# Performance work log

Measured on AMD Instinct MI355X. Metric: run time of the kernel, lower is better.

The kernel has to match this reference:

```python
import jax, jax.numpy as jnp
import numpy as np

EPS = 1e-5

def _layernorm(x, w, b):
    mu = jnp.mean(x, axis=-1, keepdims=True)
    var = jnp.var(x, axis=-1, keepdims=True)
    return (x - mu) * jax.lax.rsqrt(var + EPS) * w + b

def setup_inputs() -> dict:
    key = jax.random.key(0)
    ks = jax.random.split(key, 9)
    b, s, dim = 4, 4096, 2048
    m, n, dim_ctx = 8, 64, 1024
    heads, dim_head = 8, 64
    inner = heads * dim_head
    x = jax.random.normal(ks[0], (b, s, dim), dtype=jnp.float32)
    context = jax.random.normal(ks[1], (b, m, n, dim_ctx), dtype=jnp.float32)
    media_locations = jax.random.randint(ks[2], (b, s), 0, m, dtype=jnp.int64)
    scale = 0.02
    norm_w = jnp.ones((dim,), jnp.float32)
    norm_b = jnp.zeros((dim,), jnp.float32)
    normc_w = jnp.ones((dim_ctx,), jnp.float32)
    normc_b = jnp.zeros((dim_ctx,), jnp.float32)
    Wq = jax.random.normal(ks[3], (dim, inner), jnp.float32) * scale
    Wkv = jax.random.normal(ks[4], (dim_ctx, 2 * inner), jnp.float32) * scale
    Wout = jax.random.normal(ks[5], (inner, dim), jnp.float32) * scale
    return {"x": x, "context": context, "media_locations": media_locations,
            "norm_w": norm_w, "norm_b": norm_b, "normc_w": normc_w, "normc_b": normc_b,
            "Wq": Wq, "Wkv": Wkv, "Wout": Wout}

def reference(x, context, media_locations, norm_w, norm_b, normc_w, normc_b, Wq, Wkv, Wout):
    heads, dim_head = 8, 64
    b, m, n, dc = context.shape
    scale = dim_head ** -0.5
    xn = _layernorm(x, norm_w, norm_b)                       # [b,s,dim]
    ctx = _layernorm(context.reshape(b, m * n, dc), normc_w, normc_b)  # [b,mn,dc]
    q = xn @ Wq                                              # [b,s,inner]
    kv = ctx @ Wkv                                           # [b,mn,2*inner]
    k, v = jnp.split(kv, 2, axis=-1)
    def to_heads(t):
        return t.reshape(t.shape[0], t.shape[1], heads, dim_head).transpose(0, 2, 1, 3)
    q, k, v = to_heads(q), to_heads(k), to_heads(v)          # [b,h,*,d]
    sim = jnp.einsum('bhid,bhjd->bhij', q, k) * scale        # [b,h,s,mn]
    # image-causal mask: kv token j belongs to image j//n; query i may only
    # attend to image media_locations[b,i] (negative index => all masked)
    j_img = jnp.arange(m * n) // n                           # [mn]
    allowed = (media_locations[:, :, None] == j_img[None, None, :]) & (media_locations[:, :, None] >= 0)
    sim = jnp.where(allowed[:, None, :, :], sim, -jnp.inf)
    attn = jax.nn.softmax(sim, axis=-1)
    out = jnp.einsum('bhij,bhjd->bhid', attn, v)             # [b,h,s,d]
    out = out.transpose(0, 2, 1, 3).reshape(b, x.shape[1], heads * dim_head)
    return out @ Wout
```

## Files before the change

### kernel.cpp

```cpp
#include <hip/hip_runtime.h>

typedef unsigned short u16;
typedef unsigned int u32;
typedef __attribute__((ext_vector_type(8))) short short8;
typedef __attribute__((ext_vector_type(4))) short short4_t;
typedef __attribute__((ext_vector_type(4))) float f32x4;

__device__ __forceinline__ float bf2f(u16 u){ return __uint_as_float(((u32)u)<<16); }
__device__ __forceinline__ u16 f2bf(float f){ u32 x = __float_as_uint(f); return (u16)((x + 0x7FFFu + ((x>>16)&1u)) >> 16); }

#define OFF_FLAG   ((size_t)0)
#define OFF_COUNTS ((size_t)256)
#define OFF_LISTS  ((size_t)4096)
#define OFF_XN     ((size_t)(1<<20))
#define OFF_CTXN   (OFF_XN    + (size_t)67108864)
#define OFF_WQT    (OFF_CTXN  + (size_t)4194304)
#define OFF_WKVT   (OFF_WQT   + (size_t)2097152)
#define OFF_WOUTT  (OFF_WKVT  + (size_t)2097152)
#define OFF_Q      (OFF_WOUTT + (size_t)2097152)
#define OFF_KV     (OFF_Q     + (size_t)16777216)
#define OFF_ATTN   (OFF_KV    + (size_t)4194304)
#define OFF_VT     (OFF_ATTN  + (size_t)16777216)
#define WS_NEEDED  (OFF_VT    + (size_t)2097152)

__global__ void prep_kernel(const int* __restrict__ ml32, int* __restrict__ flag, int* __restrict__ counts){
  int t = threadIdx.x;
  if (t < 32) counts[t] = 0;
  __shared__ int nz;
  if (t == 0) nz = 0;
  __syncthreads();
  if (t < 128 && ml32[2*t+1] != 0) atomicAdd(&nz, 1);
  __syncthreads();
  if (t == 0) flag[0] = (nz == 0) ? 1 : 0;
}

template<int D>
__global__ __launch_bounds__(256) void ln_bf16(const float* __restrict__ x, const float* __restrict__ w,
                                               const float* __restrict__ b, u16* __restrict__ out){
  constexpr int VEC = D/256;
  int row = blockIdx.x;
  const float* xr = x + (size_t)row*D;
  int tid = threadIdx.x;
  float v[VEC];
  #pragma unroll
  for (int i=0;i<VEC;i+=4){
    f32x4 f = *(const f32x4*)(xr + tid*VEC + i);
    v[i]=f[0]; v[i+1]=f[1]; v[i+2]=f[2]; v[i+3]=f[3];
  }
  float s=0.f, sq=0.f;
  #pragma unroll
  for (int i=0;i<VEC;++i){ s += v[i]; sq += v[i]*v[i]; }
  #pragma unroll
  for (int off=32;off;off>>=1){ s += __shfl_xor(s,off,64); sq += __shfl_xor(sq,off,64); }
  __shared__ float red[8];
  int lane = tid&63, wid = tid>>6;
  if (lane==0){ red[wid]=s; red[4+wid]=sq; }
  __syncthreads();
  s  = red[0]+red[1]+red[2]+red[3];
  sq = red[4]+red[5]+red[6]+red[7];
  float mu = s/(float)D;
  float var = sq/(float)D - mu*mu;
  float rs = rsqrtf(var + 1e-5f);
  u16 o[VEC];
  #pragma unroll
  for (int i=0;i<VEC;i+=4){
    f32x4 wv = *(const f32x4*)(w + tid*VEC + i);
    f32x4 bv = *(const f32x4*)(b + tid*VEC + i);
    #pragma unroll
    for (int u=0;u<4;++u) o[i+u] = f2bf((v[i+u]-mu)*rs*wv[u] + bv[u]);
  }
  if constexpr (VEC==8) *(short8*)(out + (size_t)row*D + tid*8) = *(short8*)o;
  else                  *(short4_t*)(out + (size_t)row*D + tid*4) = *(short4_t*)o;
}

__global__ __launch_bounds__(256) void transpose_all(const float* __restrict__ Wq, const float* __restrict__ Wkv,
                                                     const float* __restrict__ Wout, u16* __restrict__ WqT,
                                                     u16* __restrict__ WkvT, u16* __restrict__ WoutT){
  __shared__ float t[32][33];
  int id = blockIdx.x;
  const float* in; u16* out; int K, N, tile, tx_n;
  if (id < 1024)      { in=Wq;   out=WqT;   K=2048; N=512;  tile=id;      tx_n=16; }
  else if (id < 2048) { in=Wkv;  out=WkvT;  K=1024; N=1024; tile=id-1024; tx_n=32; }
  else                { in=Wout; out=WoutT; K=512;  N=2048; tile=id-2048; tx_n=64; }
  int n0 = (tile % tx_n)*32, k0 = (tile / tx_n)*32;
  int tx = threadIdx.x & 31, ty = threadIdx.x >> 5;
  #pragma unroll
  for (int r=0;r<32;r+=8) t[ty+r][tx] = in[(size_t)(k0+ty+r)*N + n0+tx];
  __syncthreads();
  #pragma unroll
  for (int r=0;r<32;r+=8) out[(size_t)(n0+ty+r)*K + k0+tx] = f2bf(t[tx][ty+r]);
}

__global__ __launch_bounds__(256) void transpose_v(const u16* __restrict__ kvb, u16* __restrict__ vt){
  int h = blockIdx.x, bl = blockIdx.y;
  __shared__ u16 t[64][72];
  int tid = threadIdx.x;
  const u16* src = kvb + (size_t)(bl*64)*1024 + 512 + h*64;
  #pragma unroll
  for (int i=0;i<2;++i){
    int idx = i*2048 + tid*8;
    int key = idx>>6, d = idx&63;
    *(short8*)&t[key][d] = *(const short8*)(src + (size_t)key*1024 + d);
  }
  __syncthreads();
  u16* dst = vt + (size_t)(bl*8+h)*4096;
  #pragma unroll
  for (int i=0;i<2;++i){
    int idx = i*2048 + tid*8;
    int d = idx>>6, k0 = idx&63;
    u16 tmp[8];
    #pragma unroll
    for (int u=0;u<8;++u) tmp[u] = t[k0+u][d];
    *(short8*)(dst + d*64 + k0) = *(short8*)tmp;
  }
}

template<int MODE>
__global__ __launch_bounds__(256) void gemm_bt(const u16* __restrict__ A, const u16* __restrict__ B,
                                               void* __restrict__ Cv, int M, int N, int K){
  __shared__ __align__(16) u16 lds[2][2][128*32];
  int tid = threadIdx.x, lane = tid&63, wid = tid>>6;
  int nbn = N>>7;
  int nwg = gridDim.x;
  int wg = blockIdx.x;
  int cpx = nwg>>3;
  wg = (wg&7)*cpx + (wg>>3);
  int brow = wg/nbn, bcol = wg%nbn;

  auto stage = [&](int buf, int kt){
    #pragma unroll
    for (int i=0;i<2;++i){
      int cb = i*256 + wid*64;
      int c  = cb + lane;
      int row = c>>2, kc = c&3;
      const u16* ga = A + (size_t)(brow*128+row)*K + kt*32 + kc*8;
      __builtin_amdgcn_global_load_lds((const __attribute__((address_space(1))) u32*)ga,
          (__attribute__((address_space(3))) u32*)&lds[buf][0][cb*8], 16, 0, 0);
      const u16* gb = B + (size_t)(bcol*128+row)*K + kt*32 + kc*8;
      __builtin_amdgcn_global_load_lds((const __attribute__((address_space(1))) u32*)gb,
          (__attribute__((address_space(3))) u32*)&lds[buf][1][cb*8], 16, 0, 0);
    }
  };

  int wm = wid>>1, wn = wid&1;
  f32x4 acc[4][4] = {};
  int nkt = K>>5;
  stage(0,0);
  __syncthreads();
  for (int kt=0; kt<nkt; ++kt){
    int cur = kt&1;
    if (kt+1<nkt) stage(cur^1, kt+1);
    short8 af[4], bfr[4];
    int r = lane&15, kq = lane>>4;
    #pragma unroll
    for (int mi=0;mi<4;++mi) af[mi]  = *(const short8*)&lds[cur][0][(wm*64+mi*16+r)*32 + kq*8];
    #pragma unroll
    for (int ni=0;ni<4;++ni) bfr[ni] = *(const short8*)&lds[cur][1][(wn*64+ni*16+r)*32 + kq*8];
    #pragma unroll
    for (int mi=0;mi<4;++mi)
      #pragma unroll
      for (int ni=0;ni<4;++ni)
        acc[mi][ni] = __builtin_amdgcn_mfma_f32_16x16x32_bf16(af[mi], bfr[ni], acc[mi][ni], 0,0,0);
    __syncthreads();
  }
  int r4 = (lane>>4)*4, cc = lane&15;
  #pragma unroll
  for (int mi=0;mi<4;++mi)
    #pragma unroll
    for (int ni=0;ni<4;++ni)
      #pragma unroll
      for (int rr=0;rr<4;++rr){
        int row = brow*128 + wm*64 + mi*16 + r4 + rr;
        int col = bcol*128 + wn*64 + ni*16 + cc;
        float val = acc[mi][ni][rr];
        if (MODE==2) val *= 0.125f;
        if (MODE)  ((u16*)Cv)[(size_t)row*N+col] = f2bf(val);
        else       ((float*)Cv)[(size_t)row*N+col] = val;
      }
}

__global__ void bucket_kernel(const int* __restrict__ ml32, const int* __restrict__ flag,
                              int* __restrict__ counts, int* __restrict__ lists){
  int i = blockIdx.x*256 + threadIdx.x;
  int loc = flag[0] ? ml32[2*i] : ml32[i];
  int bl = (i>>12)*8 + loc;
  int pos = atomicAdd(&counts[bl], 1);
  lists[bl*4096 + pos] = i & 4095;
}

__global__ __launch_bounds__(512) void attn_mfma5(const u16* __restrict__ qb, const u16* __restrict__ kvb,
                                                  const u16* __restrict__ vt, u16* __restrict__ ob,
                                                  const int* __restrict__ counts, const int* __restrict__ lists){
  int bl = blockIdx.y, chunk = blockIdx.x;
  int cnt = counts[bl];
  int q0 = chunk*32;
  if (q0 >= cnt) return;
  int b = bl>>3, loc = bl&7;
  int tid = threadIdx.x, lane = tid&63, h = tid>>6;
  __shared__ u16 qs[32][520];
  int r = lane&15, g = lane>>4;

  const u16* kbase = kvb + (size_t)(b*512 + loc*64)*1024 + h*64;
  short8 kfr[4][2];
  #pragma unroll
  for (int nt=0;nt<4;++nt){
    const u16* krow = kbase + (size_t)(nt*16 + r)*1024;
    kfr[nt][0] = *(const short8*)(krow + g*8);
    kfr[nt][1] = *(const short8*)(krow + 32 + g*8);
  }
  const u16* vbase = vt + (size_t)(bl*8 + h)*4096;
  short8 vf[2][4];
  #pragma unroll
  for (int nt=0;nt<4;++nt){
    const u16* vrow = vbase + (size_t)(nt*16 + r)*64;
    vf[0][nt] = *(const short8*)(vrow + g*8);
    vf[1][nt] = *(const short8*)(vrow + 32 + g*8);
  }

  const u16* qbase = qb + (size_t)(b*4096)*512;
  #pragma unroll
  for (int p=0;p<4;++p){
    int c = p*512 + tid;
    int row = c>>6, cc = c&63;
    int qq = (q0 + row < cnt) ? lists[bl*4096 + q0 + row] : -1;
    if (qq >= 0)
      *(short8*)&qs[row][cc*8] = *(const short8*)(qbase + (size_t)qq*512 + cc*8);
  }
  __syncthreads();

  short8 qf[2][2];
  #pragma unroll
  for (int mt=0;mt<2;++mt){
    qf[mt][0] = *(const short8*)&qs[mt*16+r][h*64 + g*8];
    qf[mt][1] = *(const short8*)&qs[mt*16+r][h*64 + 32 + g*8];
  }

  f32x4 acc[2][4] = {};
  #pragma unroll
  for (int mt=0;mt<2;++mt)
    #pragma unroll
    for (int nt=0;nt<4;++nt){
      acc[mt][nt] = __builtin_amdgcn_mfma_f32_16x16x32_bf16(qf[mt][0], kfr[nt][0], acc[mt][nt], 0,0,0);
      acc[mt][nt] = __builtin_amdgcn_mfma_f32_16x16x32_bf16(qf[mt][1], kfr[nt][1], acc[mt][nt], 0,0,0);
    }

  #pragma unroll
  for (int mt=0;mt<2;++mt){
    #pragma unroll
    for (int rr=0;rr<4;++rr){
      float m = fmaxf(fmaxf(acc[mt][0][rr], acc[mt][1][rr]), fmaxf(acc[mt][2][rr], acc[mt][3][rr]));
      #pragma unroll
      for (int off=1;off<16;off<<=1) m = fmaxf(m, __shfl_xor(m, off));
      float e0 = __expf(acc[mt][0][rr]-m), e1 = __expf(acc[mt][1][rr]-m);
      float e2 = __expf(acc[mt][2][rr]-m), e3 = __expf(acc[mt][3][rr]-m);
      float sum = (e0+e1)+(e2+e3);
      #pragma unroll
      for (int off=1;off<16;off<<=1) sum += __shfl_xor(sum, off);
      float rs = 1.0f/sum;
      int row = mt*16 + g*4 + rr;
      qs[row][h*64 +  0 + r] = f2bf(e0*rs);
      qs[row][h*64 + 16 + r] = f2bf(e1*rs);
      qs[row][h*64 + 32 + r] = f2bf(e2*rs);
      qs[row][h*64 + 48 + r] = f2bf(e3*rs);
    }
  }

  f32x4 oacc[2][4] = {};
  #pragma unroll
  for (int mt=0;mt<2;++mt){
    short8 pa0 = *(const short8*)&qs[mt*16 + r][h*64 + g*8];
    short8 pa1 = *(const short8*)&qs[mt*16 + r][h*64 + 32 + g*8];
    #pragma unroll
    for (int nt=0;nt<4;++nt){
      oacc[mt][nt] = __builtin_amdgcn_mfma_f32_16x16x32_bf16(pa0, vf[0][nt], oacc[mt][nt], 0,0,0);
      oacc[mt][nt] = __builtin_amdgcn_mfma_f32_16x16x32_bf16(pa1, vf[1][nt], oacc[mt][nt], 0,0,0);
    }
  }

  #pragma unroll
  for (int mt=0;mt<2;++mt)
    #pragma unroll
    for (int rr=0;rr<4;++rr){
      int row = mt*16 + g*4 + rr;
      #pragma unroll
      for (int nt=0;nt<4;++nt)
        qs[row][h*64 + nt*16 + r] = f2bf(oacc[mt][nt][rr]);
    }
  __syncthreads();

  #pragma unroll
  for (int p=0;p<4;++p){
    int c = p*512 + tid;
    int row = c>>6, cc = c&63;
    int qq = (q0 + row < cnt) ? lists[bl*4096 + q0 + row] : -1;
    if (qq >= 0)
      *(short8*)(ob + ((size_t)(b*4096) + qq)*512 + cc*8) = *(const short8*)&qs[row][cc*8];
  }
}

extern "C" void kernel_launch(void* const* d_in, const int* in_sizes, int n_in,
                              void* d_out, int out_size, void* d_ws, size_t ws_size,
                              hipStream_t stream) {
  const float* x    = (const float*)d_in[0];
  const float* ctx  = (const float*)d_in[1];
  const int*   ml   = (const int*)d_in[2];
  const float* nw   = (const float*)d_in[3];
  const float* nb   = (const float*)d_in[4];
  const float* ncw  = (const float*)d_in[5];
  const float* ncb  = (const float*)d_in[6];
  const float* Wq   = (const float*)d_in[7];
  const float* Wkv  = (const float*)d_in[8];
  const float* Wout = (const float*)d_in[9];
  float* out = (float*)d_out;
  char* ws = (char*)d_ws;
  if (ws_size < WS_NEEDED) return;

  int* flag   = (int*)(ws + OFF_FLAG);
  int* counts = (int*)(ws + OFF_COUNTS);
  int* lists  = (int*)(ws + OFF_LISTS);
  u16* xn     = (u16*)(ws + OFF_XN);
  u16* ctxn   = (u16*)(ws + OFF_CTXN);
  u16* WqT    = (u16*)(ws + OFF_WQT);
  u16* WkvT   = (u16*)(ws + OFF_WKVT);
  u16* WoutT  = (u16*)(ws + OFF_WOUTT);
  u16* qbuf   = (u16*)(ws + OFF_Q);
  u16* kvbuf  = (u16*)(ws + OFF_KV);
  u16* attn_o = (u16*)(ws + OFF_ATTN);
  u16* vtbuf  = (u16*)(ws + OFF_VT);

  prep_kernel<<<1,256,0,stream>>>(ml, flag, counts);
  ln_bf16<2048><<<16384,256,0,stream>>>(x,   nw,  nb,  xn);
  ln_bf16<1024><<<2048, 256,0,stream>>>(ctx, ncw, ncb, ctxn);
  transpose_all<<<3072, 256,0,stream>>>(Wq, Wkv, Wout, WqT, WkvT, WoutT);
  gemm_bt<2><<<512, 256,0,stream>>>(xn,   WqT,  qbuf,  16384, 512,  2048);
  gemm_bt<1><<<128, 256,0,stream>>>(ctxn, WkvT, kvbuf, 2048,  1024, 1024);
  transpose_v<<<dim3(8,32),256,0,stream>>>(kvbuf, vtbuf);
  bucket_kernel<<<64,256,0,stream>>>(ml, flag, counts, lists);
  attn_mfma5<<<dim3(128,32),512,0,stream>>>(qbuf, kvbuf, vtbuf, attn_o, counts, lists);
  gemm_bt<0><<<2048,256,0,stream>>>(attn_o, WoutT, out, 16384, 2048, 512);
}
```

Baseline: 241.5 us.

## Merge small prep kernels into fewer launches and aggregate bucket atomics in LDS

Combines the context layernorm, weight transposes and flag/count init into one kernel, merges the Q and KV GEMMs into a single launch, and fuses the V transpose with bucketing. Bucketing now counts per block in shared memory before doing one global atomic per bucket. This cuts the number of launches from ten to six and removes tail bubbles from tiny grids. The cost is divergent block roles and dependence on launch ordering for the counts reset.

```diff
diff --git a/kernel.cpp b/kernel.cpp
--- a/kernel.cpp
+++ b/kernel.cpp
@@ -23,21 +23,9 @@
 #define OFF_VT     (OFF_ATTN  + (size_t)16777216)
 #define WS_NEEDED  (OFF_VT    + (size_t)2097152)
 
-__global__ void prep_kernel(const int* __restrict__ ml32, int* __restrict__ flag, int* __restrict__ counts){
-  int t = threadIdx.x;
-  if (t < 32) counts[t] = 0;
-  __shared__ int nz;
-  if (t == 0) nz = 0;
-  __syncthreads();
-  if (t < 128 && ml32[2*t+1] != 0) atomicAdd(&nz, 1);
-  __syncthreads();
-  if (t == 0) flag[0] = (nz == 0) ? 1 : 0;
-}
-
-template<int D>
-__global__ __launch_bounds__(256) void ln_bf16(const float* __restrict__ x, const float* __restrict__ w,
-                                               const float* __restrict__ b, u16* __restrict__ out){
-  constexpr int VEC = D/256;
+__global__ __launch_bounds__(256) void ln_x(const float* __restrict__ x, const float* __restrict__ w,
+                                            const float* __restrict__ b, u16* __restrict__ out){
+  constexpr int D = 2048, VEC = 8;
   int row = blockIdx.x;
   const float* xr = x + (size_t)row*D;
   int tid = threadIdx.x;
@@ -69,60 +57,72 @@
     #pragma unroll
     for (int u=0;u<4;++u) o[i+u] = f2bf((v[i+u]-mu)*rs*wv[u] + bv[u]);
   }
-  if constexpr (VEC==8) *(short8*)(out + (size_t)row*D + tid*8) = *(short8*)o;
-  else                  *(short4_t*)(out + (size_t)row*D + tid*4) = *(short4_t*)o;
-}
-
-__global__ __launch_bounds__(256) void transpose_all(const float* __restrict__ Wq, const float* __restrict__ Wkv,
-                                                     const float* __restrict__ Wout, u16* __restrict__ WqT,
-                                                     u16* __restrict__ WkvT, u16* __restrict__ WoutT){
+  *(short8*)(out + (size_t)row*D + tid*8) = *(short8*)o;
+}
+
+__global__ __launch_bounds__(256) void ctx_prep(const float* __restrict__ ctx, const float* __restrict__ ncw,
+                                                const float* __restrict__ ncb, u16* __restrict__ ctxn,
+                                                const float* __restrict__ Wq, const float* __restrict__ Wkv,
+                                                const float* __restrict__ Wout, u16* __restrict__ WqT,
+                                                u16* __restrict__ WkvT, u16* __restrict__ WoutT,
+                                                const int* __restrict__ ml32, int* __restrict__ flag,
+                                                int* __restrict__ counts){
+  int id = blockIdx.x, tid = threadIdx.x;
+  __shared__ float red[8];
   __shared__ float t[32][33];
-  int id = blockIdx.x;
-  const float* in; u16* out; int K, N, tile, tx_n;
-  if (id < 1024)      { in=Wq;   out=WqT;   K=2048; N=512;  tile=id;      tx_n=16; }
-  else if (id < 2048) { in=Wkv;  out=WkvT;  K=1024; N=1024; tile=id-1024; tx_n=32; }
-  else                { in=Wout; out=WoutT; K=512;  N=2048; tile=id-2048; tx_n=64; }
-  int n0 = (tile % tx_n)*32, k0 = (tile / tx_n)*32;
-  int tx = threadIdx.x & 31, ty = threadIdx.x >> 5;
-  #pragma unroll
-  for (int r=0;r<32;r+=8) t[ty+r][tx] = in[(size_t)(k0+ty+r)*N + n0+tx];
-  __syncthreads();
-  #pragma unroll
-  for (int r=0;r<32;r+=8) out[(size_t)(n0+ty+r)*K + k0+tx] = f2bf(t[tx][ty+r]);
-}
-
-__global__ __launch_bounds__(256) void transpose_v(const u16* __restrict__ kvb, u16* __restrict__ vt){
-  int h = blockIdx.x, bl = blockIdx.y;
-  __shared__ u16 t[64][72];
-  int tid = threadIdx.x;
-  const u16* src = kvb + (size_t)(bl*64)*1024 + 512 + h*64;
-  #pragma unroll
-  for (int i=0;i<2;++i){
-    int idx = i*2048 + tid*8;
-    int key = idx>>6, d = idx&63;
-    *(short8*)&t[key][d] = *(const short8*)(src + (size_t)key*1024 + d);
-  }
-  __syncthreads();
-  u16* dst = vt + (size_t)(bl*8+h)*4096;
-  #pragma unroll
-  for (int i=0;i<2;++i){
-    int idx = i*2048 + tid*8;
-    int d = idx>>6, k0 = idx&63;
-    u16 tmp[8];
-    #pragma unroll
-    for (int u=0;u<8;++u) tmp[u] = t[k0+u][d];
-    *(short8*)(dst + d*64 + k0) = *(short8*)tmp;
+  __shared__ int nz;
+  if (id < 2048){
+    constexpr int D = 1024;
+    const float* xr = ctx + (size_t)id*D;
+    f32x4 f = *(const f32x4*)(xr + tid*4);
+    float s = f[0]+f[1]+f[2]+f[3];
+    float sq = f[0]*f[0]+f[1]*f[1]+f[2]*f[2]+f[3]*f[3];
+    #pragma unroll
+    for (int off=32;off;off>>=1){ s += __shfl_xor(s,off,64); sq += __shfl_xor(sq,off,64); }
+    int lane = tid&63, wid = tid>>6;
+    if (lane==0){ red[wid]=s; red[4+wid]=sq; }
+    __syncthreads();
+    s  = red[0]+red[1]+red[2]+red[3];
+    sq = red[4]+red[5]+red[6]+red[7];
+    float mu = s/(float)D;
+    float var = sq/(float)D - mu*mu;
+    float rs = rsqrtf(var + 1e-5f);
+    f32x4 wv = *(const f32x4*)(ncw + tid*4);
+    f32x4 bv = *(const f32x4*)(ncb + tid*4);
+    u16 o[4];
+    #pragma unroll
+    for (int u=0;u<4;++u) o[u] = f2bf((f[u]-mu)*rs*wv[u] + bv[u]);
+    *(short4_t*)(ctxn + (size_t)id*D + tid*4) = *(short4_t*)o;
+  } else if (id < 5120){
+    int wid2 = id - 2048;
+    const float* in; u16* out; int K, N, tile, tx_n;
+    if (wid2 < 1024)      { in=Wq;   out=WqT;   K=2048; N=512;  tile=wid2;      tx_n=16; }
+    else if (wid2 < 2048) { in=Wkv;  out=WkvT;  K=1024; N=1024; tile=wid2-1024; tx_n=32; }
+    else                  { in=Wout; out=WoutT; K=512;  N=2048; tile=wid2-2048; tx_n=64; }
+    int n0 = (tile % tx_n)*32, k0 = (tile / tx_n)*32;
+    int tx = tid & 31, ty = tid >> 5;
+    #pragma unroll
+    for (int r=0;r<32;r+=8) t[ty+r][tx] = in[(size_t)(k0+ty+r)*N + n0+tx];
+    __syncthreads();
+    #pragma unroll
+    for (int r=0;r<32;r+=8) out[(size_t)(n0+ty+r)*K + k0+tx] = f2bf(t[tx][ty+r]);
+  } else {
+    if (tid < 32) counts[tid] = 0;
+    if (tid == 0) nz = 0;
+    __syncthreads();
+    if (tid < 128 && ml32[2*tid+1] != 0) atomicAdd(&nz, 1);
+    __syncthreads();
+    if (tid == 0) flag[0] = (nz == 0) ? 1 : 0;
   }
 }
 
 template<int MODE>
-__global__ __launch_bounds__(256) void gemm_bt(const u16* __restrict__ A, const u16* __restrict__ B,
-                                               void* __restrict__ Cv, int M, int N, int K){
-  __shared__ __align__(16) u16 lds[2][2][128*32];
+__device__ __forceinline__ void gemm_body(u16 (*lds)[2][128*32],
+                                          const u16* __restrict__ A, const u16* __restrict__ B,
+                                          void* __restrict__ Cv, int M, int N, int K, int wg0, int nwg){
   int tid = threadIdx.x, lane = tid&63, wid = tid>>6;
   int nbn = N>>7;
-  int nwg = gridDim.x;
-  int wg = blockIdx.x;
+  int wg = wg0;
   int cpx = nwg>>3;
   wg = (wg&7)*cpx + (wg>>3);
   int brow = wg/nbn, bcol = wg%nbn;
@@ -179,13 +179,59 @@
       }
 }
 
-__global__ void bucket_kernel(const int* __restrict__ ml32, const int* __restrict__ flag,
-                              int* __restrict__ counts, int* __restrict__ lists){
-  int i = blockIdx.x*256 + threadIdx.x;
-  int loc = flag[0] ? ml32[2*i] : ml32[i];
-  int bl = (i>>12)*8 + loc;
-  int pos = atomicAdd(&counts[bl], 1);
-  lists[bl*4096 + pos] = i & 4095;
+__global__ __launch_bounds__(256) void gemm_out(const u16* __restrict__ A, const u16* __restrict__ B,
+                                                float* __restrict__ C){
+  __shared__ __align__(16) u16 lds[2][2][128*32];
+  gemm_body<0>(lds, A, B, C, 16384, 2048, 512, blockIdx.x, gridDim.x);
+}
+
+__global__ __launch_bounds__(256) void gemm_qkv(const u16* __restrict__ xn, const u16* __restrict__ WqT,
+                                                u16* __restrict__ qbuf, const u16* __restrict__ ctxn,
+                                                const u16* __restrict__ WkvT, u16* __restrict__ kvbuf){
+  __shared__ __align__(16) u16 lds[2][2][128*32];
+  if (blockIdx.x < 512) gemm_body<2>(lds, xn,   WqT,  qbuf,  16384, 512,  2048, blockIdx.x,     512);
+  else                  gemm_body<1>(lds, ctxn, WkvT, kvbuf, 2048,  1024, 1024, blockIdx.x-512, 128);
+}
+
+__global__ __launch_bounds__(256) void tv_bucket(const u16* __restrict__ kvb, u16* __restrict__ vt,
+                                                 const int* __restrict__ ml32, const int* __restrict__ flag,
+                                                 int* __restrict__ counts, int* __restrict__ lists){
+  int h = blockIdx.x, bl = blockIdx.y;
+  int tid = threadIdx.x;
+  int bid = bl*8 + h;
+  __shared__ int lc[32], lbase[32];
+  __shared__ u16 t[64][72];
+  if (bid < 64){
+    if (tid < 32) lc[tid] = 0;
+    __syncthreads();
+    int i = bid*256 + tid;
+    int loc = flag[0] ? ml32[2*i] : ml32[i];
+    int blk = (i>>12)*8 + loc;
+    int lpos = atomicAdd(&lc[blk], 1);
+    __syncthreads();
+    if (tid < 32 && lc[tid] > 0) lbase[tid] = atomicAdd(&counts[tid], lc[tid]);
+    __syncthreads();
+    lists[blk*4096 + lbase[blk] + lpos] = i & 4095;
+    __syncthreads();
+  }
+  const u16* src = kvb + (size_t)(bl*64)*1024 + 512 + h*64;
+  #pragma unroll
+  for (int i=0;i<2;++i){
+    int idx = i*2048 + tid*8;
+    int key = idx>>6, d = idx&63;
+    *(short8*)&t[key][d] = *(const short8*)(src + (size_t)key*1024 + d);
+  }
+  __syncthreads();
+  u16* dst = vt + (size_t)(bl*8+h)*4096;
+  #pragma unroll
+  for (int i=0;i<2;++i){
+    int idx = i*2048 + tid*8;
+    int d = idx>>6, k0 = idx&63;
+    u16 tmp[8];
+    #pragma unroll
+    for (int u=0;u<8;++u) tmp[u] = t[k0+u][d];
+    *(short8*)(dst + d*64 + k0) = *(short8*)tmp;
+  }
 }
 
 __global__ __launch_bounds__(512) void attn_mfma5(const u16* __restrict__ qb, const u16* __restrict__ kvb,
@@ -328,14 +374,10 @@
   u16* attn_o = (u16*)(ws + OFF_ATTN);
   u16* vtbuf  = (u16*)(ws + OFF_VT);
 
-  prep_kernel<<<1,256,0,stream>>>(ml, flag, counts);
-  ln_bf16<2048><<<16384,256,0,stream>>>(x,   nw,  nb,  xn);
-  ln_bf16<1024><<<2048, 256,0,stream>>>(ctx, ncw, ncb, ctxn);
-  transpose_all<<<3072, 256,0,stream>>>(Wq, Wkv, Wout, WqT, WkvT, WoutT);
-  gemm_bt<2><<<512, 256,0,stream>>>(xn,   WqT,  qbuf,  16384, 512,  2048);
-  gemm_bt<1><<<128, 256,0,stream>>>(ctxn, WkvT, kvbuf, 2048,  1024, 1024);
-  transpose_v<<<dim3(8,32),256,0,stream>>>(kvbuf, vtbuf);
-  bucket_kernel<<<64,256,0,stream>>>(ml, flag, counts, lists);
+  ln_x<<<16384,256,0,stream>>>(x, nw, nb, xn);
+  ctx_prep<<<5121,256,0,stream>>>(ctx, ncw, ncb, ctxn, Wq, Wkv, Wout, WqT, WkvT, WoutT, ml, flag, counts);
+  gemm_qkv<<<640,256,0,stream>>>(xn, WqT, qbuf, ctxn, WkvT, kvbuf);
+  tv_bucket<<<dim3(8,32),256,0,stream>>>(kvbuf, vtbuf, ml, flag, counts, lists);
   attn_mfma5<<<dim3(128,32),512,0,stream>>>(qbuf, kvbuf, vtbuf, attn_o, counts, lists);
-  gemm_bt<0><<<2048,256,0,stream>>>(attn_o, WoutT, out, 16384, 2048, 512);
-}
+  gemm_out<<<2048,256,0,stream>>>(attn_o, WoutT, out);
+}
```

Result: faster. 198.0 us (-18.0%).
